# Performance work log

Measured on AMD Instinct MI355X. Metric: run time of the kernel, lower is better.

The kernel has to match this reference:

```python
import jax, jax.numpy as jnp
import numpy as np

N_NODES = 50000
BN_EPS = 1e-5


def setup_inputs() -> dict:
    key = jax.random.key(0)
    ks = jax.random.split(key, 6)
    N, E, CIN, CH, COUT = N_NODES, 800000, 128, 256, 128
    node_feat = jax.random.normal(ks[0], (N, CIN), dtype=jnp.float32)
    edge_index = jax.random.randint(ks[1], (2, E), 0, N, dtype=jnp.int64)
    # Glorot-ish init for weights
    W1 = jax.random.normal(ks[2], (CIN, CH), dtype=jnp.float32) / np.sqrt(CIN)
    b1 = jnp.zeros((CH,), dtype=jnp.float32)
    bn_gamma = jnp.ones((CH,), dtype=jnp.float32)
    bn_beta = jnp.zeros((CH,), dtype=jnp.float32)
    W2 = jax.random.normal(ks[3], (CH, COUT), dtype=jnp.float32) / np.sqrt(CH)
    b2 = jnp.zeros((COUT,), dtype=jnp.float32)
    return {"node_feat": node_feat, "edge_index": edge_index, "W1": W1, "b1": b1,
            "bn_gamma": bn_gamma, "bn_beta": bn_beta, "W2": W2, "b2": b2}


def gcn_conv(x, W, b, src, dst, n_nodes):
    """PyG GCNConv: out = D^-1/2 (A+I) D^-1/2 (x W) + b."""
    h = x @ W                                   # [N, C_out]
    loop = jnp.arange(n_nodes, dtype=src.dtype)
    src_f = jnp.concatenate([src, loop])        # self-loops appended
    dst_f = jnp.concatenate([dst, loop])
    deg = jax.ops.segment_sum(jnp.ones_like(dst_f, dtype=h.dtype), dst_f,
                              num_segments=n_nodes)
    dinv = jax.lax.rsqrt(jnp.maximum(deg, 1.0))  # deg >= 1 due to self-loops
    norm = dinv[src_f] * dinv[dst_f]             # [E+N]
    msg = h[src_f] * norm[:, None]               # gather + scale
    return jax.ops.segment_sum(msg, dst_f, num_segments=n_nodes) + b


def batch_norm(x, gamma, beta):
    mean = jnp.mean(x, axis=0)
    var = jnp.mean((x - mean) ** 2, axis=0)      # biased var (torch BN normalization)
    return (x - mean) * jax.lax.rsqrt(var + BN_EPS) * gamma + beta


def reference(node_feat, edge_index, W1, b1, bn_gamma, bn_beta, W2, b2):
    src, dst = edge_index[0], edge_index[1]
    x = gcn_conv(node_feat, W1, b1, src, dst, N_NODES)
    x = batch_norm(x, bn_gamma, bn_beta)
    x = jax.nn.relu(x)
    # dropout is identity at inference
    x = gcn_conv(x, W2, b2, src, dst, N_NODES)
    return x
```

## Files before the change

### kernel.cpp

```cpp
#include <hip/hip_runtime.h>
#include <hip/hip_fp16.h>

#define CIN 128
#define CH 256
#define COUT 128
#define BN_EPS 1e-5f

typedef __attribute__((ext_vector_type(8))) short bf16x8;
typedef __attribute__((ext_vector_type(4))) float f32x4;

__device__ __forceinline__ short f2bf(float x) {
    unsigned u = __float_as_uint(x);
    unsigned r = (u + 0x7fffu + ((u >> 16) & 1u)) >> 16;
    return (short)r;
}
__device__ __forceinline__ float bf2f(short h) {
    return __uint_as_float(((unsigned)(unsigned short)h) << 16);
}

__global__ void k_deg(const int* __restrict__ dst, int* __restrict__ degi,
                      unsigned short* __restrict__ rank, int E) {
    int e = blockIdx.x * 256 + threadIdx.x;
    if (e < E) rank[e] = (unsigned short)atomicAdd(&degi[dst[e]], 1);
}

__global__ void k_scan1(const int* __restrict__ degi, float* __restrict__ dinv,
                        int* __restrict__ blocksum, int N) {
    __shared__ int s[256];
    int i = blockIdx.x * 256 + threadIdx.x;
    int v = (i < N) ? degi[i] : 0;
    if (i < N) dinv[i] = rsqrtf((float)(v + 1));
    s[threadIdx.x] = v;
    __syncthreads();
    for (int st = 128; st > 0; st >>= 1) {
        if (threadIdx.x < st) s[threadIdx.x] += s[threadIdx.x + st];
        __syncthreads();
    }
    if (threadIdx.x == 0) blocksum[blockIdx.x] = s[0];
}

__global__ void k_scan3(const int* __restrict__ degi, const int* __restrict__ blocksum,
                        int nb, int* __restrict__ rowstart, int N, int E) {
    __shared__ int sb[256];
    __shared__ int s[256];
    int bv = (threadIdx.x < nb) ? blocksum[threadIdx.x] : 0;
    sb[threadIdx.x] = bv;
    __syncthreads();
    for (int st = 1; st < 256; st <<= 1) {
        int t = (threadIdx.x >= st) ? sb[threadIdx.x - st] : 0;
        __syncthreads();
        sb[threadIdx.x] += t;
        __syncthreads();
    }
    int boff = (blockIdx.x == 0) ? 0 : sb[blockIdx.x - 1];

    int i = blockIdx.x * 256 + threadIdx.x;
    int v = (i < N) ? degi[i] : 0;
    s[threadIdx.x] = v;
    __syncthreads();
    for (int st = 1; st < 256; st <<= 1) {
        int t = (threadIdx.x >= st) ? s[threadIdx.x - st] : 0;
        __syncthreads();
        s[threadIdx.x] += t;
        __syncthreads();
    }
    if (i < N) rowstart[i] = s[threadIdx.x] - v + boff;
    if (blockIdx.x == 0 && threadIdx.x == 0) rowstart[N] = E;
}

__global__ void k_fill(const int* __restrict__ src, const int* __restrict__ dst,
                       const unsigned short* __restrict__ rank,
                       const int* __restrict__ rowstart,
                       unsigned short* __restrict__ csr, int E) {
    int e = blockIdx.x * 256 + threadIdx.x;
    if (e >= E) return;
    int d = dst[e];
    int pos = rowstart[d] + (int)rank[e];
    __builtin_nontemporal_store((unsigned short)src[e], &csr[pos]);
}

__global__ void k_prep(const float* __restrict__ W1, const float* __restrict__ W2,
                       short* __restrict__ W1sw, short* __restrict__ W2sw,
                       const float4* __restrict__ nf, short4* __restrict__ nfb,
                       int* __restrict__ degi, float* __restrict__ stats,
                       int n4, int N) {
    int t = blockIdx.x * 256 + threadIdx.x;
    if (t < 32768) {
        if (t < 512) stats[t] = 0.0f;
        int n = t >> 7, kk = t & 127;
        float v = W1[kk * 256 + n];
        int t16 = n >> 4, m = n & 15;
        int ks = kk >> 5, q = (kk >> 3) & 3, j = kk & 7;
        W1sw[(t16 * 4 + ks) * 512 + (q * 16 + m) * 8 + j] = f2bf(v);
    } else if (t < 65536) {
        int u = t - 32768;
        int n = u >> 8, kk = u & 255;
        float v = W2[kk * 128 + n];
        int t16 = n >> 4, m = n & 15;
        int ks = kk >> 5, q = (kk >> 3) & 3, j = kk & 7;
        W2sw[(t16 * 8 + ks) * 512 + (q * 16 + m) * 8 + j] = f2bf(v);
    } else {
        int u = t - 65536;
        if (u < n4) {
            float4 v = nf[u];
            short4 s;
            s.x = f2bf(v.x); s.y = f2bf(v.y); s.z = f2bf(v.z); s.w = f2bf(v.w);
            nfb[u] = s;
        } else {
            int u2 = u - n4;
            if (u2 < N) degi[u2] = 0;
        }
    }
}

template <int MODE>
__global__ __launch_bounds__(256) void k_gather(const short* __restrict__ xb,
                                                const int* __restrict__ rowstart,
                                                const unsigned short* __restrict__ csr,
                                                const float* __restrict__ dinv,
                                                const float* __restrict__ bias,
                                                float* __restrict__ out,
                                                short* __restrict__ ob, int N) {
    int t = blockIdx.x * 256 + threadIdx.x;
    int r = t >> 4;
    int c = t & 15;
    if (r >= N) return;
    float di = dinv[r];
    float w0 = di * di;
    bf16x8 sv = *(const bf16x8*)(xb + (size_t)r * 128 + c * 8);
    float acc[8];
    #pragma unroll
    for (int j = 0; j < 8; ++j) acc[j] = bf2f(sv[j]) * w0;
    int e0 = rowstart[r], e1 = rowstart[r + 1];
    int e = e0;
    for (; e + 7 < e1; e += 8) {
        int s[8];
        #pragma unroll
        for (int i = 0; i < 8; ++i) s[i] = csr[e + i];
        float w[8];
        #pragma unroll
        for (int i = 0; i < 8; ++i) w[i] = dinv[s[i]] * di;
        bf16x8 x[8];
        #pragma unroll
        for (int i = 0; i < 8; ++i) x[i] = *(const bf16x8*)(xb + (size_t)s[i] * 128 + c * 8);
        #pragma unroll
        for (int i = 0; i < 8; ++i)
            #pragma unroll
            for (int j = 0; j < 8; ++j) acc[j] = fmaf(w[i], bf2f(x[i][j]), acc[j]);
    }
    for (; e + 3 < e1; e += 4) {
        int s[4];
        #pragma unroll
        for (int i = 0; i < 4; ++i) s[i] = csr[e + i];
        float w[4];
        #pragma unroll
        for (int i = 0; i < 4; ++i) w[i] = dinv[s[i]] * di;
        bf16x8 x[4];
        #pragma unroll
        for (int i = 0; i < 4; ++i) x[i] = *(const bf16x8*)(xb + (size_t)s[i] * 128 + c * 8);
        #pragma unroll
        for (int i = 0; i < 4; ++i)
            #pragma unroll
            for (int j = 0; j < 8; ++j) acc[j] = fmaf(w[i], bf2f(x[i][j]), acc[j]);
    }
    for (; e < e1; ++e) {
        int s0 = csr[e];
        float ww = dinv[s0] * di;
        bf16x8 x0 = *(const bf16x8*)(xb + (size_t)s0 * 128 + c * 8);
        #pragma unroll
        for (int j = 0; j < 8; ++j) acc[j] = fmaf(ww, bf2f(x0[j]), acc[j]);
    }
    if (MODE == 0) {
        bf16x8 h;
        #pragma unroll
        for (int j = 0; j < 8; ++j) h[j] = f2bf(acc[j]);
        *(bf16x8*)(ob + (size_t)r * 128 + c * 8) = h;
    } else {
        float4 b0 = *(const float4*)(bias + c * 8);
        float4 b1 = *(const float4*)(bias + c * 8 + 4);
        float4 o0 = make_float4(acc[0] + b0.x, acc[1] + b0.y, acc[2] + b0.z, acc[3] + b0.w);
        float4 o1 = make_float4(acc[4] + b1.x, acc[5] + b1.y, acc[6] + b1.z, acc[7] + b1.w);
        *(float4*)(out + (size_t)r * 128 + c * 8) = o0;
        *(float4*)(out + (size_t)r * 128 + c * 8 + 4) = o1;
    }
}

__device__ __forceinline__ bf16x8 bnrelu8(bf16x8 raw, const float* __restrict__ scsh, int c) {
    float4 sc0 = *(const float4*)(scsh + c);
    float4 sc1 = *(const float4*)(scsh + c + 4);
    float4 sh0 = *(const float4*)(scsh + 256 + c);
    float4 sh1 = *(const float4*)(scsh + 256 + c + 4);
    bf16x8 o;
    o[0] = f2bf(fmaxf(fmaf(bf2f(raw[0]), sc0.x, sh0.x), 0.f));
    o[1] = f2bf(fmaxf(fmaf(bf2f(raw[1]), sc0.y, sh0.y), 0.f));
    o[2] = f2bf(fmaxf(fmaf(bf2f(raw[2]), sc0.z, sh0.z), 0.f));
    o[3] = f2bf(fmaxf(fmaf(bf2f(raw[3]), sc0.w, sh0.w), 0.f));
    o[4] = f2bf(fmaxf(fmaf(bf2f(raw[4]), sc1.x, sh1.x), 0.f));
    o[5] = f2bf(fmaxf(fmaf(bf2f(raw[5]), sc1.y, sh1.y), 0.f));
    o[6] = f2bf(fmaxf(fmaf(bf2f(raw[6]), sc1.z, sh1.z), 0.f));
    o[7] = f2bf(fmaxf(fmaf(bf2f(raw[7]), sc1.w, sh1.w), 0.f));
    return o;
}

template <int K, int NOUT, bool STATS, bool BIAS, bool BNRELU>
__global__ __launch_bounds__(256, 4) void k_gemm(const short* __restrict__ A,
                                                 const short* __restrict__ Bsw,
                                                 const float* __restrict__ bias,
                                                 const float* __restrict__ scsh,
                                                 short* __restrict__ C,
                                                 float* __restrict__ partials, int M) {
    constexpr int CT = NOUT / 64;
    constexpr int KS = K / 32;
    constexpr int KP = K + 8;
    constexpr int LROW = NOUT + 8;
    constexpr int LSZ = (64 * KP > 64 * LROW) ? 64 * KP : 64 * LROW;
    __shared__ __align__(16) short lds[LSZ];
    int tid = threadIdx.x;
    int wave = tid >> 6;
    int lane = tid & 63;
    int m = lane & 15;
    int q = lane >> 4;
    int row0 = blockIdx.x * 64;

    constexpr int CPRA = K / 8;
    #pragma unroll
    for (int i = 0; i < (64 * CPRA) / 256; ++i) {
        int idx = i * 256 + tid;
        int r = idx / CPRA, cc = idx % CPRA;
        int gr = row0 + r;
        if (gr >= M) gr = M - 1;
        bf16x8 v = *(const bf16x8*)(A + (size_t)gr * K + cc * 8);
        if (BNRELU) v = bnrelu8(v, scsh, cc * 8);
        *(bf16x8*)(lds + r * KP + cc * 8) = v;
    }
    __syncthreads();

    f32x4 acc[4][CT];
    #pragma unroll
    for (int rt = 0; rt < 4; ++rt)
        #pragma unroll
        for (int ct = 0; ct < CT; ++ct)
            acc[rt][ct] = (f32x4){0.f, 0.f, 0.f, 0.f};

    #pragma unroll
    for (int ks = 0; ks < KS; ++ks) {
        bf16x8 bh[CT];
        #pragma unroll
        for (int ct = 0; ct < CT; ++ct)
            bh[ct] = *(const bf16x8*)(Bsw + (size_t)((wave * CT + ct) * KS + ks) * 512 + lane * 8);
        bf16x8 af[4];
        #pragma unroll
        for (int rt = 0; rt < 4; ++rt)
            af[rt] = *(const bf16x8*)(lds + (rt * 16 + m) * KP + ks * 32 + q * 8);
        #pragma unroll
        for (int ct = 0; ct < CT; ++ct)
            #pragma unroll
            for (int rt = 0; rt < 4; ++rt)
                acc[rt][ct] = __builtin_amdgcn_mfma_f32_16x16x32_bf16(af[rt], bh[ct], acc[rt][ct], 0, 0, 0);
    }
    __syncthreads();

    #pragma unroll
    for (int ct = 0; ct < CT; ++ct) {
        int col = wave * (NOUT / 4) + ct * 16 + m;
        float bv = BIAS ? bias[col] : 0.f;
        float s = 0.f, sq = 0.f;
        #pragma unroll
        for (int rt = 0; rt < 4; ++rt) {
            #pragma unroll
            for (int r = 0; r < 4; ++r) {
                int lrow = rt * 16 + q * 4 + r;
                float v = acc[rt][ct][r] + bv;
                if (STATS && row0 + lrow < M) { s += v; sq = fmaf(v, v, sq); }
                lds[lrow * LROW + col] = f2bf(v);
            }
        }
        if (STATS) {
            s += __shfl_xor(s, 16, 64);
            s += __shfl_xor(s, 32, 64);
            sq += __shfl_xor(sq, 16, 64);
            sq += __shfl_xor(sq, 32, 64);
            if (lane < 16) {
                partials[(size_t)blockIdx.x * 512 + col] = s;
                partials[(size_t)blockIdx.x * 512 + 256 + col] = sq;
            }
        }
    }
    __syncthreads();
    constexpr int CPR = NOUT / 8;
    #pragma unroll
    for (int i = 0; i < (64 * CPR) / 256; ++i) {
        int idx = i * 256 + tid;
        int row = idx / CPR;
        int ch = idx % CPR;
        if (row0 + row < M)
            *(bf16x8*)(C + (size_t)(row0 + row) * NOUT + ch * 8) =
                *(const bf16x8*)(lds + row * LROW + ch * 8);
    }
}

__global__ void k_redstats(const float* __restrict__ partials, float* __restrict__ stats,
                           int nb, int rpb) {
    int sid = threadIdx.x;
    int r0 = blockIdx.x * rpb;
    int r1 = r0 + rpb;
    if (r1 > nb) r1 = nb;
    float acc = 0.f;
    for (int r = r0; r < r1; ++r) acc += partials[(size_t)r * 512 + sid];
    unsafeAtomicAdd(&stats[sid], acc);
}

__global__ void k_bnfinal(const float* __restrict__ stats, const float* __restrict__ gamma,
                          const float* __restrict__ beta, float* __restrict__ scsh, int N) {
    int c = threadIdx.x;
    float invN = 1.0f / (float)N;
    float mean = stats[c] * invN;
    float var = stats[256 + c] * invN - mean * mean;
    var = fmaxf(var, 0.f);
    float inv = rsqrtf(var + BN_EPS);
    float sc = gamma[c] * inv;
    scsh[c] = sc;
    scsh[256 + c] = fmaf(-mean, sc, beta[c]);
}

extern "C" void kernel_launch(void* const* d_in, const int* in_sizes, int n_in,
                              void* d_out, int out_size, void* d_ws, size_t ws_size,
                              hipStream_t stream) {
    const float* nf    = (const float*)d_in[0];
    const int*   ei    = (const int*)d_in[1];
    const float* W1    = (const float*)d_in[2];
    const float* b1    = (const float*)d_in[3];
    const float* gamma = (const float*)d_in[4];
    const float* beta  = (const float*)d_in[5];
    const float* W2    = (const float*)d_in[6];
    const float* b2    = (const float*)d_in[7];
    float* out = (float*)d_out;

    const int N = in_sizes[0] / CIN;
    const int E = in_sizes[1] / 2;
    const int* src = ei;
    const int* dst = ei + E;

    const int nb1 = (N + 63) / 64;

    char* ws = (char*)d_ws;
    auto align256 = [](size_t x) { return (x + 255) & ~(size_t)255; };
    size_t off = 0;
    int*   degi = (int*)(ws + off);      off += align256((size_t)N * 4);
    float* stats = (float*)(ws + off);   off += align256(512 * 4);
    float* dinv = (float*)(ws + off);    off += align256((size_t)N * 4);
    int*   rowstart = (int*)(ws + off);  off += align256((size_t)(N + 1) * 4);
    int*   blocksum = (int*)(ws + off);  off += align256(256 * 4);
    float* scsh = (float*)(ws + off);    off += align256(512 * 4);
    short* W1sw = (short*)(ws + off);    off += align256(32768 * 2);
    short* W2sw = (short*)(ws + off);    off += align256(32768 * 2);
    float* partials = (float*)(ws + off); off += align256((size_t)nb1 * 512 * 4);
    unsigned short* rank = (unsigned short*)(ws + off); off += align256((size_t)E * 2);
    unsigned short* csr = (unsigned short*)(ws + off);  off += align256((size_t)E * 2);
    short* nfb = (short*)(ws + off);     off += align256((size_t)N * CIN * 2);
    short* agg1b = (short*)(ws + off);   off += align256((size_t)N * CIN * 2);
    short* x1b = (short*)(ws + off);     off += align256((size_t)N * CH * 2);
    short* yb = (short*)(ws + off);      off += align256((size_t)N * COUT * 2);

    int nbN = (N + 255) / 256;
    int nbE = (E + 255) / 256;
    int n4 = N * 32;

    k_prep<<<(65536 + n4 + N + 255) / 256, 256, 0, stream>>>(
        W1, W2, W1sw, W2sw, (const float4*)nf, (short4*)nfb, degi, stats, n4, N);

    k_deg<<<nbE, 256, 0, stream>>>(dst, degi, rank, E);
    k_scan1<<<nbN, 256, 0, stream>>>(degi, dinv, blocksum, N);
    k_scan3<<<nbN, 256, 0, stream>>>(degi, blocksum, nbN, rowstart, N, E);
    k_fill<<<nbE, 256, 0, stream>>>(src, dst, rank, rowstart, csr, E);

    k_gather<0><<<(N * 16 + 255) / 256, 256, 0, stream>>>(
        nfb, rowstart, csr, dinv, nullptr, nullptr, agg1b, N);

    k_gemm<CIN, CH, true, true, false><<<nb1, 256, 0, stream>>>(
        agg1b, W1sw, b1, nullptr, x1b, partials, N);

    {
        int rblocks = 8;
        int rpb = (nb1 + rblocks - 1) / rblocks;
        k_redstats<<<rblocks, 512, 0, stream>>>(partials, stats, nb1, rpb);
    }
    k_bnfinal<<<1, 256, 0, stream>>>(stats, gamma, beta, scsh, N);

    k_gemm<CH, COUT, false, false, true><<<nb1, 256, 0, stream>>>(
        x1b, W2sw, nullptr, scsh, yb, nullptr, N);

    k_gather<1><<<(N * 16 + 255) / 256, 256, 0, stream>>>(
        yb, rowstart, csr, dinv, b2, out, nullptr, N);
}
```

Baseline: 266.6 us.

## Fuse first gather into GEMM1, sort rows by degree, fold BN stats into GEMM

Computes a degree histogram and a degree-sorted row permutation, then fuses the layer-1 neighbor aggregation directly into the first MFMA GEMM through LDS, removing the agg1b intermediate buffer and one launch. BN statistics are accumulated with atomics in GEMM1 and the BN scale/shift is computed inside GEMM2, removing the redstats and bnfinal kernels. Both gathers process rows in descending degree order to balance work across waves. The cost is atomic contention on the stats array and scattered writes through the permutation, and the gather inside GEMM1 may limit occupancy.

```diff
diff --git a/kernel.cpp b/kernel.cpp
--- a/kernel.cpp
+++ b/kernel.cpp
@@ -1,5 +1,4 @@
 #include <hip/hip_runtime.h>
-#include <hip/hip_fp16.h>
 
 #define CIN 128
 #define CH 256
@@ -18,6 +17,51 @@
     return __uint_as_float(((unsigned)(unsigned short)h) << 16);
 }
 
+__device__ __forceinline__ void gather_edges(const short* __restrict__ xb,
+                                             const unsigned short* __restrict__ csr,
+                                             const float* __restrict__ dinv,
+                                             int e0, int e1, float di, int c,
+                                             float* acc) {
+    int e = e0;
+    for (; e + 7 < e1; e += 8) {
+        int s[8];
+        #pragma unroll
+        for (int i = 0; i < 8; ++i) s[i] = csr[e + i];
+        float w[8];
+        #pragma unroll
+        for (int i = 0; i < 8; ++i) w[i] = dinv[s[i]] * di;
+        bf16x8 x[8];
+        #pragma unroll
+        for (int i = 0; i < 8; ++i) x[i] = *(const bf16x8*)(xb + (size_t)s[i] * 128 + c * 8);
+        #pragma unroll
+        for (int i = 0; i < 8; ++i)
+            #pragma unroll
+            for (int j = 0; j < 8; ++j) acc[j] = fmaf(w[i], bf2f(x[i][j]), acc[j]);
+    }
+    for (; e + 3 < e1; e += 4) {
+        int s[4];
+        #pragma unroll
+        for (int i = 0; i < 4; ++i) s[i] = csr[e + i];
+        float w[4];
+        #pragma unroll
+        for (int i = 0; i < 4; ++i) w[i] = dinv[s[i]] * di;
+        bf16x8 x[4];
+        #pragma unroll
+        for (int i = 0; i < 4; ++i) x[i] = *(const bf16x8*)(xb + (size_t)s[i] * 128 + c * 8);
+        #pragma unroll
+        for (int i = 0; i < 4; ++i)
+            #pragma unroll
+            for (int j = 0; j < 8; ++j) acc[j] = fmaf(w[i], bf2f(x[i][j]), acc[j]);
+    }
+    for (; e < e1; ++e) {
+        int s0 = csr[e];
+        float ww = dinv[s0] * di;
+        bf16x8 x0 = *(const bf16x8*)(xb + (size_t)s0 * 128 + c * 8);
+        #pragma unroll
+        for (int j = 0; j < 8; ++j) acc[j] = fmaf(ww, bf2f(x0[j]), acc[j]);
+    }
+}
+
 __global__ void k_deg(const int* __restrict__ dst, int* __restrict__ degi,
                       unsigned short* __restrict__ rank, int E) {
     int e = blockIdx.x * 256 + threadIdx.x;
@@ -25,68 +69,104 @@
 }
 
 __global__ void k_scan1(const int* __restrict__ degi, float* __restrict__ dinv,
-                        int* __restrict__ blocksum, int N) {
+                        int* __restrict__ blocksum, int* __restrict__ hist, int N) {
     __shared__ int s[256];
-    int i = blockIdx.x * 256 + threadIdx.x;
+    __shared__ int h[256];
+    int tid = threadIdx.x;
+    h[tid] = 0;
+    int i = blockIdx.x * 256 + tid;
     int v = (i < N) ? degi[i] : 0;
     if (i < N) dinv[i] = rsqrtf((float)(v + 1));
-    s[threadIdx.x] = v;
-    __syncthreads();
+    s[tid] = v;
+    __syncthreads();
+    if (i < N) atomicAdd(&h[v > 255 ? 255 : v], 1);
     for (int st = 128; st > 0; st >>= 1) {
-        if (threadIdx.x < st) s[threadIdx.x] += s[threadIdx.x + st];
-        __syncthreads();
-    }
-    if (threadIdx.x == 0) blocksum[blockIdx.x] = s[0];
+        if (tid < st) s[tid] += s[tid + st];
+        __syncthreads();
+    }
+    if (tid == 0) blocksum[blockIdx.x] = s[0];
+    int hv = h[tid];
+    if (hv) atomicAdd(&hist[tid], hv);
 }
 
 __global__ void k_scan3(const int* __restrict__ degi, const int* __restrict__ blocksum,
-                        int nb, int* __restrict__ rowstart, int N, int E) {
+                        int nb, int* __restrict__ rowstart,
+                        const int* __restrict__ hist, int* __restrict__ histbase,
+                        int N, int E) {
     __shared__ int sb[256];
     __shared__ int s[256];
-    int bv = (threadIdx.x < nb) ? blocksum[threadIdx.x] : 0;
-    sb[threadIdx.x] = bv;
+    int tid = threadIdx.x;
+    int bv = (tid < nb) ? blocksum[tid] : 0;
+    sb[tid] = bv;
     __syncthreads();
     for (int st = 1; st < 256; st <<= 1) {
-        int t = (threadIdx.x >= st) ? sb[threadIdx.x - st] : 0;
-        __syncthreads();
-        sb[threadIdx.x] += t;
+        int t = (tid >= st) ? sb[tid - st] : 0;
+        __syncthreads();
+        sb[tid] += t;
         __syncthreads();
     }
     int boff = (blockIdx.x == 0) ? 0 : sb[blockIdx.x - 1];
 
-    int i = blockIdx.x * 256 + threadIdx.x;
+    int i = blockIdx.x * 256 + tid;
     int v = (i < N) ? degi[i] : 0;
-    s[threadIdx.x] = v;
+    s[tid] = v;
     __syncthreads();
     for (int st = 1; st < 256; st <<= 1) {
-        int t = (threadIdx.x >= st) ? s[threadIdx.x - st] : 0;
-        __syncthreads();
-        s[threadIdx.x] += t;
-        __syncthreads();
-    }
-    if (i < N) rowstart[i] = s[threadIdx.x] - v + boff;
-    if (blockIdx.x == 0 && threadIdx.x == 0) rowstart[N] = E;
-}
-
-__global__ void k_fill(const int* __restrict__ src, const int* __restrict__ dst,
-                       const unsigned short* __restrict__ rank,
-                       const int* __restrict__ rowstart,
-                       unsigned short* __restrict__ csr, int E) {
-    int e = blockIdx.x * 256 + threadIdx.x;
-    if (e >= E) return;
-    int d = dst[e];
-    int pos = rowstart[d] + (int)rank[e];
-    __builtin_nontemporal_store((unsigned short)src[e], &csr[pos]);
+        int t = (tid >= st) ? s[tid - st] : 0;
+        __syncthreads();
+        s[tid] += t;
+        __syncthreads();
+    }
+    if (i < N) rowstart[i] = s[tid] - v + boff;
+    if (blockIdx.x == 0 && tid == 0) rowstart[N] = E;
+
+    if (blockIdx.x == 0) {
+        __shared__ int hh[256];
+        int own = hist[tid];
+        hh[tid] = own;
+        __syncthreads();
+        for (int st = 1; st < 256; st <<= 1) {
+            int t = (tid >= st) ? hh[tid - st] : 0;
+            __syncthreads();
+            hh[tid] += t;
+            __syncthreads();
+        }
+        histbase[tid] = hh[tid] - own;
+    }
+}
+
+__global__ void k_fillperm(const int* __restrict__ src, const int* __restrict__ dst,
+                           const unsigned short* __restrict__ rank,
+                           const int* __restrict__ rowstart,
+                           unsigned short* __restrict__ csr,
+                           const int* __restrict__ degi,
+                           const int* __restrict__ histbase, int* __restrict__ histcnt,
+                           int* __restrict__ perm, int E, int N) {
+    int t = blockIdx.x * 256 + threadIdx.x;
+    if (t < E) {
+        int d = dst[t];
+        int pos = rowstart[d] + (int)rank[t];
+        __builtin_nontemporal_store((unsigned short)src[t], &csr[pos]);
+    } else {
+        int i = t - E;
+        if (i < N) {
+            int d = degi[i];
+            if (d > 255) d = 255;
+            int pos = histbase[d] + atomicAdd(&histcnt[d], 1);
+            perm[pos] = i;
+        }
+    }
 }
 
 __global__ void k_prep(const float* __restrict__ W1, const float* __restrict__ W2,
                        short* __restrict__ W1sw, short* __restrict__ W2sw,
                        const float4* __restrict__ nf, short4* __restrict__ nfb,
                        int* __restrict__ degi, float* __restrict__ stats,
-                       int n4, int N) {
+                       int* __restrict__ hist, int n4, int N) {
     int t = blockIdx.x * 256 + threadIdx.x;
     if (t < 32768) {
         if (t < 512) stats[t] = 0.0f;
+        else if (t < 1024) hist[t - 512] = 0;
         int n = t >> 7, kk = t & 127;
         float v = W1[kk * 256 + n];
         int t16 = n >> 4, m = n & 15;
@@ -113,75 +193,112 @@
     }
 }
 
-template <int MODE>
-__global__ __launch_bounds__(256) void k_gather(const short* __restrict__ xb,
-                                                const int* __restrict__ rowstart,
-                                                const unsigned short* __restrict__ csr,
-                                                const float* __restrict__ dinv,
-                                                const float* __restrict__ bias,
-                                                float* __restrict__ out,
-                                                short* __restrict__ ob, int N) {
-    int t = blockIdx.x * 256 + threadIdx.x;
-    int r = t >> 4;
-    int c = t & 15;
-    if (r >= N) return;
-    float di = dinv[r];
-    float w0 = di * di;
-    bf16x8 sv = *(const bf16x8*)(xb + (size_t)r * 128 + c * 8);
-    float acc[8];
-    #pragma unroll
-    for (int j = 0; j < 8; ++j) acc[j] = bf2f(sv[j]) * w0;
-    int e0 = rowstart[r], e1 = rowstart[r + 1];
-    int e = e0;
-    for (; e + 7 < e1; e += 8) {
-        int s[8];
-        #pragma unroll
-        for (int i = 0; i < 8; ++i) s[i] = csr[e + i];
-        float w[8];
-        #pragma unroll
-        for (int i = 0; i < 8; ++i) w[i] = dinv[s[i]] * di;
-        bf16x8 x[8];
-        #pragma unroll
-        for (int i = 0; i < 8; ++i) x[i] = *(const bf16x8*)(xb + (size_t)s[i] * 128 + c * 8);
-        #pragma unroll
-        for (int i = 0; i < 8; ++i)
-            #pragma unroll
-            for (int j = 0; j < 8; ++j) acc[j] = fmaf(w[i], bf2f(x[i][j]), acc[j]);
-    }
-    for (; e + 3 < e1; e += 4) {
-        int s[4];
-        #pragma unroll
-        for (int i = 0; i < 4; ++i) s[i] = csr[e + i];
-        float w[4];
-        #pragma unroll
-        for (int i = 0; i < 4; ++i) w[i] = dinv[s[i]] * di;
-        bf16x8 x[4];
-        #pragma unroll
-        for (int i = 0; i < 4; ++i) x[i] = *(const bf16x8*)(xb + (size_t)s[i] * 128 + c * 8);
-        #pragma unroll
-        for (int i = 0; i < 4; ++i)
-            #pragma unroll
-            for (int j = 0; j < 8; ++j) acc[j] = fmaf(w[i], bf2f(x[i][j]), acc[j]);
-    }
-    for (; e < e1; ++e) {
-        int s0 = csr[e];
-        float ww = dinv[s0] * di;
-        bf16x8 x0 = *(const bf16x8*)(xb + (size_t)s0 * 128 + c * 8);
-        #pragma unroll
-        for (int j = 0; j < 8; ++j) acc[j] = fmaf(ww, bf2f(x0[j]), acc[j]);
-    }
-    if (MODE == 0) {
+__global__ __launch_bounds__(256, 4) void k_gemm1g(
+        const short* __restrict__ xb, const int* __restrict__ rowstart,
+        const unsigned short* __restrict__ csr, const float* __restrict__ dinv,
+        const int* __restrict__ perm, const short* __restrict__ Bsw,
+        const float* __restrict__ bias, short* __restrict__ C,
+        float* __restrict__ stats, int M) {
+    constexpr int K = CIN, NOUT = CH;
+    constexpr int CT = NOUT / 64;
+    constexpr int KS = K / 32;
+    constexpr int KP = K + 8;
+    constexpr int LROW = NOUT + 8;
+    constexpr int LSZ = (64 * KP > 64 * LROW) ? 64 * KP : 64 * LROW;
+    __shared__ __align__(16) short lds[LSZ];
+    __shared__ int prow[64];
+    int tid = threadIdx.x;
+    int wave = tid >> 6;
+    int lane = tid & 63;
+    int m = lane & 15;
+    int q = lane >> 4;
+    int row0 = blockIdx.x * 64;
+    if (tid < 64) {
+        int pos = row0 + tid;
+        if (pos >= M) pos = M - 1;
+        prow[tid] = perm[M - 1 - pos];
+    }
+    __syncthreads();
+
+    int c = tid & 15;
+    int g = tid >> 4;
+    #pragma unroll
+    for (int p = 0; p < 4; ++p) {
+        int rl = p * 16 + g;
+        int r = prow[rl];
+        float di = dinv[r];
+        float w0 = di * di;
+        bf16x8 sv = *(const bf16x8*)(xb + (size_t)r * 128 + c * 8);
+        float acc[8];
+        #pragma unroll
+        for (int j = 0; j < 8; ++j) acc[j] = bf2f(sv[j]) * w0;
+        gather_edges(xb, csr, dinv, rowstart[r], rowstart[r + 1], di, c, acc);
         bf16x8 h;
         #pragma unroll
         for (int j = 0; j < 8; ++j) h[j] = f2bf(acc[j]);
-        *(bf16x8*)(ob + (size_t)r * 128 + c * 8) = h;
-    } else {
-        float4 b0 = *(const float4*)(bias + c * 8);
-        float4 b1 = *(const float4*)(bias + c * 8 + 4);
-        float4 o0 = make_float4(acc[0] + b0.x, acc[1] + b0.y, acc[2] + b0.z, acc[3] + b0.w);
-        float4 o1 = make_float4(acc[4] + b1.x, acc[5] + b1.y, acc[6] + b1.z, acc[7] + b1.w);
-        *(float4*)(out + (size_t)r * 128 + c * 8) = o0;
-        *(float4*)(out + (size_t)r * 128 + c * 8 + 4) = o1;
+        *(bf16x8*)(lds + rl * KP + c * 8) = h;
+    }
+    __syncthreads();
+
+    f32x4 acc4[4][CT];
+    #pragma unroll
+    for (int rt = 0; rt < 4; ++rt)
+        #pragma unroll
+        for (int ct = 0; ct < CT; ++ct)
+            acc4[rt][ct] = (f32x4){0.f, 0.f, 0.f, 0.f};
+
+    #pragma unroll
+    for (int ks = 0; ks < KS; ++ks) {
+        bf16x8 bh[CT];
+        #pragma unroll
+        for (int ct = 0; ct < CT; ++ct)
+            bh[ct] = *(const bf16x8*)(Bsw + (size_t)((wave * CT + ct) * KS + ks) * 512 + lane * 8);
+        bf16x8 af[4];
+        #pragma unroll
+        for (int rt = 0; rt < 4; ++rt)
+            af[rt] = *(const bf16x8*)(lds + (rt * 16 + m) * KP + ks * 32 + q * 8);
+        #pragma unroll
+        for (int ct = 0; ct < CT; ++ct)
+            #pragma unroll
+            for (int rt = 0; rt < 4; ++rt)
+                acc4[rt][ct] = __builtin_amdgcn_mfma_f32_16x16x32_bf16(af[rt], bh[ct], acc4[rt][ct], 0, 0, 0);
+    }
+    __syncthreads();
+
+    #pragma unroll
+    for (int ct = 0; ct < CT; ++ct) {
+        int col = wave * (NOUT / 4) + ct * 16 + m;
+        float bv = bias[col];
+        float s = 0.f, sq = 0.f;
+        #pragma unroll
+        for (int rt = 0; rt < 4; ++rt) {
+            #pragma unroll
+            for (int r = 0; r < 4; ++r) {
+                int lrow = rt * 16 + q * 4 + r;
+                float v = acc4[rt][ct][r] + bv;
+                if (row0 + lrow < M) { s += v; sq = fmaf(v, v, sq); }
+                lds[lrow * LROW + col] = f2bf(v);
+            }
+        }
+        s += __shfl_xor(s, 16, 64);
+        s += __shfl_xor(s, 32, 64);
+        sq += __shfl_xor(sq, 16, 64);
+        sq += __shfl_xor(sq, 32, 64);
+        if (lane < 16) {
+            unsafeAtomicAdd(&stats[col], s);
+            unsafeAtomicAdd(&stats[256 + col], sq);
+        }
+    }
+    __syncthreads();
+    constexpr int CPR = NOUT / 8;
+    #pragma unroll
+    for (int i = 0; i < (64 * CPR) / 256; ++i) {
+        int idx = i * 256 + tid;
+        int row = idx / CPR;
+        int ch = idx % CPR;
+        if (row0 + row < M)
+            *(bf16x8*)(C + (size_t)prow[row] * NOUT + ch * 8) =
+                *(const bf16x8*)(lds + row * LROW + ch * 8);
     }
 }
 
@@ -202,19 +319,18 @@
     return o;
 }
 
-template <int K, int NOUT, bool STATS, bool BIAS, bool BNRELU>
-__global__ __launch_bounds__(256, 4) void k_gemm(const short* __restrict__ A,
-                                                 const short* __restrict__ Bsw,
-                                                 const float* __restrict__ bias,
-                                                 const float* __restrict__ scsh,
-                                                 short* __restrict__ C,
-                                                 float* __restrict__ partials, int M) {
+__global__ __launch_bounds__(256, 4) void k_gemm2(
+        const short* __restrict__ A, const short* __restrict__ Bsw,
+        const float* __restrict__ stats, const float* __restrict__ gamma,
+        const float* __restrict__ beta, short* __restrict__ C, int M) {
+    constexpr int K = CH, NOUT = COUT;
     constexpr int CT = NOUT / 64;
     constexpr int KS = K / 32;
     constexpr int KP = K + 8;
     constexpr int LROW = NOUT + 8;
     constexpr int LSZ = (64 * KP > 64 * LROW) ? 64 * KP : 64 * LROW;
     __shared__ __align__(16) short lds[LSZ];
+    __shared__ float scsh[512];
     int tid = threadIdx.x;
     int wave = tid >> 6;
     int lane = tid & 63;
@@ -222,6 +338,17 @@
     int q = lane >> 4;
     int row0 = blockIdx.x * 64;
 
+    if (tid < 256) {
+        float invN = 1.0f / (float)M;
+        float mean = stats[tid] * invN;
+        float var = fmaxf(stats[256 + tid] * invN - mean * mean, 0.f);
+        float inv = rsqrtf(var + BN_EPS);
+        float sc = gamma[tid] * inv;
+        scsh[tid] = sc;
+        scsh[256 + tid] = fmaf(-mean, sc, beta[tid]);
+    }
+    __syncthreads();
+
     constexpr int CPRA = K / 8;
     #pragma unroll
     for (int i = 0; i < (64 * CPRA) / 256; ++i) {
@@ -230,7 +357,7 @@
         int gr = row0 + r;
         if (gr >= M) gr = M - 1;
         bf16x8 v = *(const bf16x8*)(A + (size_t)gr * K + cc * 8);
-        if (BNRELU) v = bnrelu8(v, scsh, cc * 8);
+        v = bnrelu8(v, scsh, cc * 8);
         *(bf16x8*)(lds + r * KP + cc * 8) = v;
     }
     __syncthreads();
@@ -263,26 +390,12 @@
     #pragma unroll
     for (int ct = 0; ct < CT; ++ct) {
         int col = wave * (NOUT / 4) + ct * 16 + m;
-        float bv = BIAS ? bias[col] : 0.f;
-        float s = 0.f, sq = 0.f;
         #pragma unroll
         for (int rt = 0; rt < 4; ++rt) {
             #pragma unroll
             for (int r = 0; r < 4; ++r) {
                 int lrow = rt * 16 + q * 4 + r;
-                float v = acc[rt][ct][r] + bv;
-                if (STATS && row0 + lrow < M) { s += v; sq = fmaf(v, v, sq); }
-                lds[lrow * LROW + col] = f2bf(v);
-            }
-        }
-        if (STATS) {
-            s += __shfl_xor(s, 16, 64);
-            s += __shfl_xor(s, 32, 64);
-            sq += __shfl_xor(sq, 16, 64);
-            sq += __shfl_xor(sq, 32, 64);
-            if (lane < 16) {
-                partials[(size_t)blockIdx.x * 512 + col] = s;
-                partials[(size_t)blockIdx.x * 512 + 256 + col] = sq;
+                lds[lrow * LROW + col] = f2bf(acc[rt][ct][r]);
             }
         }
     }
@@ -299,28 +412,29 @@
     }
 }
 
-__global__ void k_redstats(const float* __restrict__ partials, float* __restrict__ stats,
-                           int nb, int rpb) {
-    int sid = threadIdx.x;
-    int r0 = blockIdx.x * rpb;
-    int r1 = r0 + rpb;
-    if (r1 > nb) r1 = nb;
-    float acc = 0.f;
-    for (int r = r0; r < r1; ++r) acc += partials[(size_t)r * 512 + sid];
-    unsafeAtomicAdd(&stats[sid], acc);
-}
-
-__global__ void k_bnfinal(const float* __restrict__ stats, const float* __restrict__ gamma,
-                          const float* __restrict__ beta, float* __restrict__ scsh, int N) {
-    int c = threadIdx.x;
-    float invN = 1.0f / (float)N;
-    float mean = stats[c] * invN;
-    float var = stats[256 + c] * invN - mean * mean;
-    var = fmaxf(var, 0.f);
-    float inv = rsqrtf(var + BN_EPS);
-    float sc = gamma[c] * inv;
-    scsh[c] = sc;
-    scsh[256 + c] = fmaf(-mean, sc, beta[c]);
+__global__ __launch_bounds__(256) void k_gather1(
+        const short* __restrict__ yb, const int* __restrict__ rowstart,
+        const unsigned short* __restrict__ csr, const float* __restrict__ dinv,
+        const int* __restrict__ perm, const float* __restrict__ bias,
+        float* __restrict__ out, int N) {
+    int t = blockIdx.x * 256 + threadIdx.x;
+    int sp = t >> 4;
+    int c = t & 15;
+    if (sp >= N) return;
+    int r = perm[N - 1 - sp];
+    float di = dinv[r];
+    float w0 = di * di;
+    bf16x8 sv = *(const bf16x8*)(yb + (size_t)r * 128 + c * 8);
+    float acc[8];
+    #pragma unroll
+    for (int j = 0; j < 8; ++j) acc[j] = bf2f(sv[j]) * w0;
+    gather_edges(yb, csr, dinv, rowstart[r], rowstart[r + 1], di, c, acc);
+    float4 b0 = *(const float4*)(bias + c * 8);
+    float4 b1 = *(const float4*)(bias + c * 8 + 4);
+    float4 o0 = make_float4(acc[0] + b0.x, acc[1] + b0.y, acc[2] + b0.z, acc[3] + b0.w);
+    float4 o1 = make_float4(acc[4] + b1.x, acc[5] + b1.y, acc[6] + b1.z, acc[7] + b1.w);
+    *(float4*)(out + (size_t)r * 128 + c * 8) = o0;
+    *(float4*)(out + (size_t)r * 128 + c * 8 + 4) = o1;
 }
 
 extern "C" void kernel_launch(void* const* d_in, const int* in_sizes, int n_in,
@@ -351,14 +465,14 @@
     float* dinv = (float*)(ws + off);    off += align256((size_t)N * 4);
     int*   rowstart = (int*)(ws + off);  off += align256((size_t)(N + 1) * 4);
     int*   blocksum = (int*)(ws + off);  off += align256(256 * 4);
-    float* scsh = (float*)(ws + off);    off += align256(512 * 4);
+    int*   hist = (int*)(ws + off);      off += align256(512 * 4);
+    int*   histbase = (int*)(ws + off);  off += align256(256 * 4);
+    int*   perm = (int*)(ws + off);      off += align256((size_t)N * 4);
     short* W1sw = (short*)(ws + off);    off += align256(32768 * 2);
     short* W2sw = (short*)(ws + off);    off += align256(32768 * 2);
-    float* partials = (float*)(ws + off); off += align256((size_t)nb1 * 512 * 4);
     unsigned short* rank = (unsigned short*)(ws + off); off += align256((size_t)E * 2);
     unsigned short* csr = (unsigned short*)(ws + off);  off += align256((size_t)E * 2);
     short* nfb = (short*)(ws + off);     off += align256((size_t)N * CIN * 2);
-    short* agg1b = (short*)(ws + off);   off += align256((size_t)N * CIN * 2);
     short* x1b = (short*)(ws + off);     off += align256((size_t)N * CH * 2);
     short* yb = (short*)(ws + off);      off += align256((size_t)N * COUT * 2);
 
@@ -367,29 +481,18 @@
     int n4 = N * 32;
 
     k_prep<<<(65536 + n4 + N + 255) / 256, 256, 0, stream>>>(
-        W1, W2, W1sw, W2sw, (const float4*)nf, (short4*)nfb, degi, stats, n4, N);
+        W1, W2, W1sw, W2sw, (const float4*)nf, (short4*)nfb, degi, stats, hist, n4, N);
 
     k_deg<<<nbE, 256, 0, stream>>>(dst, degi, rank, E);
-    k_scan1<<<nbN, 256, 0, stream>>>(degi, dinv, blocksum, N);
-    k_scan3<<<nbN, 256, 0, stream>>>(degi, blocksum, nbN, rowstart, N, E);
-    k_fill<<<nbE, 256, 0, stream>>>(src, dst, rank, rowstart, csr, E);
-
-    k_gather<0><<<(N * 16 + 255) / 256, 256, 0, stream>>>(
-        nfb, rowstart, csr, dinv, nullptr, nullptr, agg1b, N);
-
-    k_gemm<CIN, CH, true, true, false><<<nb1, 256, 0, stream>>>(
-        agg1b, W1sw, b1, nullptr, x1b, partials, N);
-
-    {
-        int rblocks = 8;
-        int rpb = (nb1 + rblocks - 1) / rblocks;
-        k_redstats<<<rblocks, 512, 0, stream>>>(partials, stats, nb1, rpb);
-    }
-    k_bnfinal<<<1, 256, 0, stream>>>(stats, gamma, beta, scsh, N);
-
-    k_gemm<CH, COUT, false, false, true><<<nb1, 256, 0, stream>>>(
-        x1b, W2sw, nullptr, scsh, yb, nullptr, N);
-
-    k_gather<1><<<(N * 16 + 255) / 256, 256, 0, stream>>>(
-        yb, rowstart, csr, dinv, b2, out, nullptr, N);
-}
+    k_scan1<<<nbN, 256, 0, stream>>>(degi, dinv, blocksum, hist, N);
+    k_scan3<<<nbN, 256, 0, stream>>>(degi, blocksum, nbN, rowstart, hist, histbase, N, E);
+    k_fillperm<<<(E + N + 255) / 256, 256, 0, stream>>>(
+        src, dst, rank, rowstart, csr, degi, histbase, hist + 256, perm, E, N);
+
+    k_gemm1g<<<nb1, 256, 0, stream>>>(nfb, rowstart, csr, dinv, perm, W1sw, b1, x1b, stats, N);
+
+    k_gemm2<<<nb1, 256, 0, stream>>>(x1b, W2sw, stats, gamma, beta, yb, N);
+
+    k_gather1<<<(N * 16 + 255) / 256, 256, 0, stream>>>(
+        yb, rowstart, csr, dinv, perm, b2, out, N);
+}
```

Result: slower. 369.7 us (+38.7%).
